# Optimization experiments

Hardware: AMD Instinct MI355X
Metric: run time of the kernel (lower is better)

## Reference

```python
import jax, jax.numpy as jnp
import numpy as np
import math

# Temporal Patch Shift, pattern 'C' (ratio=1 -> all heads shifted).
# torch.roll(x, s, dim=t): out[t] = x[(t - s) % T]
_SHIFT_TABLE_C = np.array([[-4, 1, 2],
                           [-1, 0, 3],
                           [-2, -3, 4]], dtype=np.int32)  # s[i%3, j%3]

def patch_shift_c(feat, inv):
    # feat: (b, T, nW, H, ws, ws, c)
    T, ws = feat.shape[1], feat.shape[4]
    s = jnp.asarray(_SHIFT_TABLE_C)[jnp.arange(ws) % 3][:, jnp.arange(ws) % 3]  # (ws, ws)
    if inv:
        s = -s
    t = jnp.arange(T)
    idx = (t[:, None, None] - s[None, :, :]) % T                 # (T, ws, ws)
    idx = idx[None, :, None, None, :, :, None]                   # bcast to feat rank
    return jnp.take_along_axis(feat, jnp.broadcast_to(idx, feat.shape), axis=1)


def _rel_pos_index(Wd, Wh, Ww):
    coords = np.stack(np.meshgrid(np.arange(Wd), np.arange(Wh), np.arange(Ww), indexing='ij'))
    cf = coords.reshape(3, -1)
    rel = (cf[:, :, None] - cf[:, None, :]).transpose(1, 2, 0).astype(np.int64)
    rel[..., 0] += Wd - 1; rel[..., 1] += Wh - 1; rel[..., 2] += Ww - 1
    rel[..., 0] *= (2 * Wh - 1) * (2 * Ww - 1)
    rel[..., 1] *= (2 * Ww - 1)
    return rel.sum(-1)  # (N, N)


def setup_inputs() -> dict:
    key = jax.random.key(0)
    ks = jax.random.split(key, 5)
    DIM, H = 512, 16
    Wd, Wh, Ww = 1, 7, 7
    N = Wd * Wh * Ww
    B_, bs, fl = 4096, 4, 16  # B_ = bs * fl * 64 windows
    x = jax.random.normal(ks[0], (B_, N, DIM), dtype=jnp.float32)
    qkv_w = jax.random.normal(ks[1], (3 * DIM, DIM), dtype=jnp.float32) * (DIM ** -0.5)
    proj_w = jax.random.normal(ks[2], (DIM, DIM), dtype=jnp.float32) * (DIM ** -0.5)
    proj_b = jnp.zeros((DIM,), dtype=jnp.float32)
    rel_bias_table = jax.random.normal(ks[3], ((2 * Wd - 1) * (2 * Wh - 1) * (2 * Ww - 1), H), dtype=jnp.float32) * 0.02
    rel_index = jnp.asarray(_rel_pos_index(Wd, Wh, Ww), dtype=jnp.int32)
    return {"x": x, "qkv_w": qkv_w, "proj_w": proj_w, "proj_b": proj_b,
            "rel_bias_table": rel_bias_table, "rel_index": rel_index,
            "batch_size": bs, "frame_len": fl}


def reference(x, qkv_w, proj_w, proj_b, rel_bias_table, rel_index, batch_size, frame_len):
    B_, N, C = x.shape
    H = rel_bias_table.shape[-1]
    c = C // H
    ws = int(math.sqrt(N))
    nW = B_ // (batch_size * frame_len)
    scale = c ** -0.5

    qkv = (x @ qkv_w.T).reshape(B_, N, 3, H, c).transpose(2, 0, 3, 1, 4)  # (3, B_, H, N, c)
    q, k, v = qkv[0], qkv[1], qkv[2]

    def shift(t, inv):
        f = t.reshape(batch_size, frame_len, nW, H, ws, ws, c)
        return patch_shift_c(f, inv).reshape(B_, H, N, c)

    q, k, v = shift(q, False), shift(k, False), shift(v, False)

    attn = jnp.einsum('bhnc,bhmc->bhnm', q * scale, k)            # (B_, H, N, N)
    bias = rel_bias_table[rel_index.reshape(-1)].reshape(N, N, H).transpose(2, 0, 1)
    attn = jax.nn.softmax(attn + bias[None], axis=-1)
    out = jnp.einsum('bhnm,bhmc->bhnc', attn, v)                  # (B_, H, N, c)
    out = shift(out, True)                                        # inverse shift back
    out = out.transpose(0, 2, 1, 3).reshape(B_, N, C)
    return out @ proj_w.T + proj_b
```

## Files before the change

kernel.cpp:

```cpp
#include <hip/hip_runtime.h>
#include <stdint.h>

typedef unsigned short u16;
typedef __attribute__((ext_vector_type(8))) short bfrag8;
typedef __attribute__((ext_vector_type(4))) float f32x4;

#define DEV static __device__ __forceinline__

DEV u16 f2bf(float f) {
  uint32_t u = __float_as_uint(f);
  u += 0x7fffu + ((u >> 16) & 1u);
  return (u16)(u >> 16);
}

DEV void async_lds16(const void* g, void* l) {
  const __attribute__((address_space(1))) uint32_t* gp =
      (const __attribute__((address_space(1))) uint32_t*)(uintptr_t)g;
  __attribute__((address_space(3))) uint32_t* lp =
      (__attribute__((address_space(3))) uint32_t*)(uint32_t)(uintptr_t)l;
  __builtin_amdgcn_global_load_lds(gp, lp, 16, 0, 0);
}

DEV int shift_of(int n) {
  int i = n / 7, j = n - i * 7;
  int idx = (i % 3) * 3 + (j % 3);
  return (int)((0x812743650ull >> (4 * idx)) & 15ull) - 4;
}

__global__ void k_f32_to_bf16(const float* __restrict__ src, u16* __restrict__ dst, int n4) {
  int i = blockIdx.x * blockDim.x + threadIdx.x;
  const int stride = gridDim.x * blockDim.x;
  for (; i < n4; i += stride) {
    float4 v = ((const float4*)src)[i];
    union { u16 h[4]; uint2 u; } o;
    o.h[0] = f2bf(v.x); o.h[1] = f2bf(v.y); o.h[2] = f2bf(v.z); o.h[3] = f2bf(v.w);
    ((uint2*)dst)[i] = o.u;
  }
}

__global__ void k_bias_pre(const float* __restrict__ tab, const int* __restrict__ ridx,
                           float* __restrict__ bp) {
  int nm = blockIdx.x * blockDim.x + threadIdx.x;
  if (nm < 2401) {
    int idx = ridx[nm];
#pragma unroll
    for (int h = 0; h < 16; ++h) bp[h * 2401 + nm] = tab[idx * 16 + h];
  }
}

template <int OUT_F32>
__global__ __launch_bounds__(256) void k_gemm_bt(const u16* __restrict__ A,
                                                 const u16* __restrict__ B,
                                                 void* __restrict__ Cp,
                                                 const float* __restrict__ bias,
                                                 int M, int N, int K) {
  __shared__ __align__(16) u16 As[4096];
  __shared__ __align__(16) u16 Bs[4096];
  const int tid = threadIdx.x;
  const int wave = tid >> 6, lane = tid & 63;
  const int quad = lane >> 4, l16 = lane & 15;
  const int wm = ((wave >> 1) & 1) << 6;
  const int wn = (wave & 1) << 6;
  const int bm = blockIdx.x, bn = blockIdx.y;

  f32x4 acc[4][4] = {};

  const int srow = lane >> 2;
  const int scol = (lane & 3) << 3;
  const u16* ga = A + (long)(bm * 128 + srow) * K + scol;
  const u16* gb = B + (long)(bn * 128 + srow) * K + scol;
  const long rstep = (long)16 * K;

  for (int k0 = 0; k0 < K; k0 += 32) {
#pragma unroll
    for (int tt = 0; tt < 2; ++tt) {
      const int region = wave * 2 + tt;
      async_lds16(ga + region * rstep + k0, &As[region * 512]);
      async_lds16(gb + region * rstep + k0, &Bs[region * 512]);
    }
    __syncthreads();
    bfrag8 af[4], bq[4];
#pragma unroll
    for (int mt = 0; mt < 4; ++mt)
      af[mt] = *(const bfrag8*)&As[(wm + mt * 16 + l16) * 32 + quad * 8];
#pragma unroll
    for (int nt = 0; nt < 4; ++nt)
      bq[nt] = *(const bfrag8*)&Bs[(wn + nt * 16 + l16) * 32 + quad * 8];
#pragma unroll
    for (int mt = 0; mt < 4; ++mt)
#pragma unroll
      for (int nt = 0; nt < 4; ++nt)
        acc[mt][nt] = __builtin_amdgcn_mfma_f32_16x16x32_bf16(af[mt], bq[nt], acc[mt][nt], 0, 0, 0);
    __syncthreads();
  }

#pragma unroll
  for (int nt = 0; nt < 4; ++nt) {
    const int col = (bn << 7) + wn + nt * 16 + l16;
    float bv = 0.f;
    if (OUT_F32) bv = bias[col];
#pragma unroll
    for (int mt = 0; mt < 4; ++mt)
#pragma unroll
      for (int i = 0; i < 4; ++i) {
        const long row = (long)(bm << 7) + wm + mt * 16 + quad * 4 + i;
        const float v = acc[mt][nt][i] + bv;
        if (OUT_F32) ((float*)Cp)[row * N + col] = v;
        else         ((u16*)Cp)[row * N + col] = f2bf(v);
      }
  }
}

__global__ __launch_bounds__(256) void k_attn(const u16* __restrict__ qkv,
                                              const float* __restrict__ bias_pre,
                                              u16* __restrict__ out_pre) {
  __shared__ __align__(16) u16 smem[4][6144];
  const int tid = threadIdx.x;
  const int wave = tid >> 6, lane = tid & 63;
  const int quad = lane >> 4, l16 = lane & 15;

  const int unit = (blockIdx.x << 2) + wave;
  const int h = unit & 15;
  const int bflat = unit >> 4;
  const int w = bflat & 63;
  const int t = (bflat >> 6) & 15;
  const int b = bflat >> 10;

  u16* qs = &smem[wave][0];
  u16* ks = &smem[wave][2048];
  u16* vt = &smem[wave][4096];
  u16* ps = &smem[wave][0];

#pragma unroll
  for (int it = 0; it < 8; ++it) {
    int idx = it * 64 + lane;
    vt[(idx >> 4) * 64 + 48 + (idx & 15)] = 0;
  }

  const int r_off = lane >> 2;
  const int ch8 = (lane & 3) << 3;

#pragma unroll
  for (int pass = 0; pass < 4; ++pass) {
    int r = pass * 16 + r_off;
    int rc = r > 48 ? 48 : r;
    int ts = (t - shift_of(rc) + 16) & 15;
    long row = ((long)((b * 16 + ts) * 64 + w)) * 49 + rc;
    const u16* gq = qkv + row * 1536 + h * 32 + ch8;
    async_lds16(gq, qs + pass * 512);
    async_lds16(gq + 512, ks + pass * 512);
  }
#pragma unroll
  for (int pass = 0; pass < 4; ++pass) {
    int r = pass * 16 + r_off;
    if (r < 49) {
      int ts = (t - shift_of(r) + 16) & 15;
      long row = ((long)((b * 16 + ts) * 64 + w)) * 49 + r;
      uint4 d = *(const uint4*)(qkv + row * 1536 + 1024 + h * 32 + ch8);
      const u16* pd = (const u16*)&d;
#pragma unroll
      for (int jj = 0; jj < 8; ++jj) vt[(ch8 + jj) * 64 + r] = pd[jj];
    }
  }

  __builtin_amdgcn_s_waitcnt(0);
  __builtin_amdgcn_sched_barrier(0);

  bfrag8 aq[4], bk[4];
#pragma unroll
  for (int tn = 0; tn < 4; ++tn) aq[tn] = *(const bfrag8*)&qs[(tn * 16 + l16) * 32 + quad * 8];
#pragma unroll
  for (int tm = 0; tm < 4; ++tm) bk[tm] = *(const bfrag8*)&ks[(tm * 16 + l16) * 32 + quad * 8];

  f32x4 s[4][4] = {};
#pragma unroll
  for (int tn = 0; tn < 4; ++tn)
#pragma unroll
    for (int tm = 0; tm < 4; ++tm)
      s[tn][tm] = __builtin_amdgcn_mfma_f32_16x16x32_bf16(aq[tn], bk[tm], s[tn][tm], 0, 0, 0);

  const float scale = 0.17677669529663687f;
#pragma unroll
  for (int tm = 0; tm < 4; ++tm) {
    const int col = tm * 16 + l16;
    const bool valid = col < 49;
    const float* bp = bias_pre + h * 2401 + col;
#pragma unroll
    for (int tn = 0; tn < 4; ++tn)
#pragma unroll
      for (int i = 0; i < 4; ++i) {
        const int row = tn * 16 + quad * 4 + i;
        const int rowc = row > 48 ? 48 : row;
        s[tn][tm][i] = valid ? (s[tn][tm][i] * scale + bp[rowc * 49]) : -1e30f;
      }
  }

  float rinv[4][4];
#pragma unroll
  for (int tn = 0; tn < 4; ++tn) {
#pragma unroll
    for (int i = 0; i < 4; ++i) {
      float m = fmaxf(fmaxf(s[tn][0][i], s[tn][1][i]), fmaxf(s[tn][2][i], s[tn][3][i]));
      m = fmaxf(m, __shfl_xor(m, 1));
      m = fmaxf(m, __shfl_xor(m, 2));
      m = fmaxf(m, __shfl_xor(m, 4));
      m = fmaxf(m, __shfl_xor(m, 8));
      float l = 0.f;
#pragma unroll
      for (int tm = 0; tm < 4; ++tm) {
        float p = __expf(s[tn][tm][i] - m);
        l += p;
        ps[(tn * 16 + quad * 4 + i) * 64 + tm * 16 + l16] = f2bf(p);
      }
      l += __shfl_xor(l, 1);
      l += __shfl_xor(l, 2);
      l += __shfl_xor(l, 4);
      l += __shfl_xor(l, 8);
      rinv[tn][i] = 1.0f / l;
    }
  }

  f32x4 o[4][2] = {};
#pragma unroll
  for (int kt = 0; kt < 2; ++kt) {
    bfrag8 ap[4], bv[2];
#pragma unroll
    for (int tn = 0; tn < 4; ++tn)
      ap[tn] = *(const bfrag8*)&ps[(tn * 16 + l16) * 64 + kt * 32 + quad * 8];
#pragma unroll
    for (int ct = 0; ct < 2; ++ct)
      bv[ct] = *(const bfrag8*)&vt[(ct * 16 + l16) * 64 + kt * 32 + quad * 8];
#pragma unroll
    for (int tn = 0; tn < 4; ++tn)
#pragma unroll
      for (int ct = 0; ct < 2; ++ct)
        o[tn][ct] = __builtin_amdgcn_mfma_f32_16x16x32_bf16(ap[tn], bv[ct], o[tn][ct], 0, 0, 0);
  }

#pragma unroll
  for (int tn = 0; tn < 4; ++tn)
#pragma unroll
    for (int i = 0; i < 4; ++i) {
      const int row = tn * 16 + quad * 4 + i;
      if (row < 49) {
        const int ts = (t - shift_of(row) + 16) & 15;
        const long fd = (long)((b * 16 + ts) * 64 + w);
        const long base = (fd * 49 + row) * 512 + h * 32;
        const float r = rinv[tn][i];
        out_pre[base + l16]      = f2bf(o[tn][0][i] * r);
        out_pre[base + 16 + l16] = f2bf(o[tn][1][i] * r);
      }
    }
}

extern "C" void kernel_launch(void* const* d_in, const int* in_sizes, int n_in,
                              void* d_out, int out_size, void* d_ws, size_t ws_size,
                              hipStream_t stream) {
  const float* x       = (const float*)d_in[0];
  const float* qkv_w   = (const float*)d_in[1];
  const float* proj_w  = (const float*)d_in[2];
  const float* proj_b  = (const float*)d_in[3];
  const float* rel_tab = (const float*)d_in[4];
  const int*   rel_idx = (const int*)d_in[5];

  const long M = 200704;
  char* ws = (char*)d_ws;
  u16*   x_bf     = (u16*)ws;
  u16*   qkvw_bf  = (u16*)(ws + 205520896);
  u16*   projw_bf = (u16*)(ws + 205520896 + 1572864);
  float* bias_pre = (float*)(ws + 205520896 + 1572864 + 524288);
  u16*   qkv_buf  = (u16*)(ws + 205520896 + 1572864 + 524288 + 262144);

  k_f32_to_bf16<<<4096, 256, 0, stream>>>(x, x_bf, (int)(M * 512 / 4));
  k_f32_to_bf16<<<768, 256, 0, stream>>>(qkv_w, qkvw_bf, 1536 * 512 / 4);
  k_f32_to_bf16<<<256, 256, 0, stream>>>(proj_w, projw_bf, 512 * 512 / 4);
  k_bias_pre<<<10, 256, 0, stream>>>(rel_tab, rel_idx, bias_pre);

  dim3 g1(1568, 12);
  k_gemm_bt<0><<<g1, 256, 0, stream>>>(x_bf, qkvw_bf, (void*)qkv_buf, nullptr, (int)M, 1536, 512);

  u16* attn_out = x_bf;
  k_attn<<<16384, 256, 0, stream>>>(qkv_buf, bias_pre, attn_out);

  dim3 g2(1568, 4);
  k_gemm_bt<1><<<g2, 256, 0, stream>>>(attn_out, projw_bf, d_out, proj_b, (int)M, 512, 512);
}
```

Before: 1.897 ms.

## Replace GEMM with 256x256 double-buffered 8-wave pipelined kernel

Replaces the 128x128 single-buffer GEMM used for the QKV and output projections with a 256x256-tile, 512-thread kernel. It uses double-buffered LDS with async global-to-LDS loads interleaved between MFMA phases, an XOR-swizzled LDS layout to avoid bank conflicts, s_setprio around MFMA bursts, and an XCD-aware block remapping. The aim is to hide load latency and raise reuse per LDS byte. In exchange it needs 128 KB of LDS and a large accumulator register footprint, which could limit occupancy.

```diff
diff --git a/kernel.cpp b/kernel.cpp
--- a/kernel.cpp
+++ b/kernel.cpp
@@ -26,6 +26,8 @@
   int idx = (i % 3) * 3 + (j % 3);
   return (int)((0x812743650ull >> (4 * idx)) & 15ull) - 4;
 }
+
+#define FENCE asm volatile("" ::: "memory")
 
 __global__ void k_f32_to_bf16(const float* __restrict__ src, u16* __restrict__ dst, int n4) {
   int i = blockIdx.x * blockDim.x + threadIdx.x;
@@ -48,67 +50,121 @@
   }
 }
 
-template <int OUT_F32>
-__global__ __launch_bounds__(256) void k_gemm_bt(const u16* __restrict__ A,
-                                                 const u16* __restrict__ B,
-                                                 void* __restrict__ Cp,
-                                                 const float* __restrict__ bias,
-                                                 int M, int N, int K) {
-  __shared__ __align__(16) u16 As[4096];
-  __shared__ __align__(16) u16 Bs[4096];
+template <int OUT_F32, int NBN>
+__global__ __launch_bounds__(512, 2) void k_gemm8(const u16* __restrict__ A,
+                                                  const u16* __restrict__ B,
+                                                  void* __restrict__ Cp,
+                                                  const float* __restrict__ bias,
+                                                  int M, int N, int K, int nwg) {
+  (void)M;
+  __shared__ __align__(16) u16 lds[65536];
   const int tid = threadIdx.x;
   const int wave = tid >> 6, lane = tid & 63;
   const int quad = lane >> 4, l16 = lane & 15;
-  const int wm = ((wave >> 1) & 1) << 6;
-  const int wn = (wave & 1) << 6;
-  const int bm = blockIdx.x, bn = blockIdx.y;
-
-  f32x4 acc[4][4] = {};
-
-  const int srow = lane >> 2;
-  const int scol = (lane & 3) << 3;
-  const u16* ga = A + (long)(bm * 128 + srow) * K + scol;
-  const u16* gb = B + (long)(bn * 128 + srow) * K + scol;
-  const long rstep = (long)16 * K;
-
-  for (int k0 = 0; k0 < K; k0 += 32) {
-#pragma unroll
-    for (int tt = 0; tt < 2; ++tt) {
-      const int region = wave * 2 + tt;
-      async_lds16(ga + region * rstep + k0, &As[region * 512]);
-      async_lds16(gb + region * rstep + k0, &Bs[region * 512]);
+  const int wm = wave >> 2, wn = wave & 3;
+
+  const int cpx = nwg >> 3;
+  const int wg = ((int)blockIdx.x & 7) * cpx + ((int)blockIdx.x >> 3);
+  const int bn = wg % NBN, bm = wg / NBN;
+
+  const int r8 = tid >> 3;
+  const int cu = (((tid & 7) ^ (r8 & 7)) << 3);
+  const u16* gA = A + (long)(bm * 256 + r8) * K + cu;
+  const u16* gB = B + (long)(bn * 256 + r8) * K + cu;
+  const long istep = (long)64 * K;
+  const long hstep = (long)128 * K;
+
+#define STAGE_A(t, h) do { const u16* g_ = gA + (h) * hstep + (t) * 64; \
+    u16* l_ = &lds[(((t) & 1) << 15) + ((h) << 13) + (wave << 9)]; \
+    async_lds16(g_, l_); async_lds16(g_ + istep, l_ + 4096); } while (0)
+#define STAGE_B(t, h) do { const u16* g_ = gB + (h) * hstep + (t) * 64; \
+    u16* l_ = &lds[(((t) & 1) << 15) + 16384 + ((h) << 13) + (wave << 9)]; \
+    async_lds16(g_, l_); async_lds16(g_ + istep, l_ + 4096); } while (0)
+
+  const int c0 = (quad << 3) ^ ((l16 & 7) << 3);
+  const int arow = (wm << 6) + l16;
+  const int brow = (wn << 5) + l16;
+
+#define LOADS_A(t, mh) do { const int cb_ = ((t) & 1) << 15; \
+    _Pragma("unroll") for (int a_ = 0; a_ < 4; ++a_) { \
+      const int ro_ = cb_ + ((((mh) << 7) + (a_ << 4) + arow) << 6); \
+      fa[a_ * 2 + 0] = *(const bfrag8*)&lds[ro_ + c0]; \
+      fa[a_ * 2 + 1] = *(const bfrag8*)&lds[ro_ + (c0 ^ 32)]; } } while (0)
+#define LOADS_B(t, nh) do { const int cb_ = (((t) & 1) << 15) + 16384; \
+    _Pragma("unroll") for (int b_ = 0; b_ < 2; ++b_) { \
+      const int ro_ = cb_ + ((((nh) << 7) + (b_ << 4) + brow) << 6); \
+      fb[((nh) * 2 + b_) * 2 + 0] = *(const bfrag8*)&lds[ro_ + c0]; \
+      fb[((nh) * 2 + b_) * 2 + 1] = *(const bfrag8*)&lds[ro_ + (c0 ^ 32)]; } } while (0)
+#define MFMA8(mh, nh) do { \
+    __builtin_amdgcn_s_setprio(1); \
+    _Pragma("unroll") for (int a_ = 0; a_ < 4; ++a_) \
+    _Pragma("unroll") for (int b_ = 0; b_ < 2; ++b_) { \
+      f32x4& c_ = acc[(mh) * 4 + a_][(nh) * 2 + b_]; \
+      c_ = __builtin_amdgcn_mfma_f32_16x16x32_bf16(fa[a_ * 2 + 0], fb[((nh) * 2 + b_) * 2 + 0], c_, 0, 0, 0); \
+      c_ = __builtin_amdgcn_mfma_f32_16x16x32_bf16(fa[a_ * 2 + 1], fb[((nh) * 2 + b_) * 2 + 1], c_, 0, 0, 0); } \
+    __builtin_amdgcn_s_setprio(0); } while (0)
+#define BAR do { FENCE; __builtin_amdgcn_s_barrier(); FENCE; } while (0)
+
+  f32x4 acc[8][4] = {};
+  bfrag8 fa[8], fb[8];
+
+  STAGE_A(0, 0); STAGE_B(0, 0); STAGE_A(0, 1); STAGE_B(0, 1);
+  STAGE_A(1, 0); STAGE_B(1, 0);
+  asm volatile("s_waitcnt vmcnt(4)" ::: "memory");
+  __builtin_amdgcn_s_barrier();
+  FENCE;
+
+  const int nIter = K >> 7;
+  for (int I = 0; I < nIter; ++I) {
+    const int t0 = I * 2, t1 = t0 + 1, t2 = t0 + 2, t3 = t0 + 3;
+    const bool more = (I + 1) < nIter;
+    LOADS_A(t0, 0); LOADS_B(t0, 0);
+    STAGE_A(t1, 1);
+    BAR; MFMA8(0, 0); BAR;
+    LOADS_B(t0, 1);
+    STAGE_B(t1, 1);
+    BAR; MFMA8(0, 1); BAR;
+    LOADS_A(t0, 1);
+    if (more) STAGE_A(t2, 0);
+    BAR; MFMA8(1, 0); BAR;
+    if (more) { STAGE_B(t2, 0); asm volatile("s_waitcnt vmcnt(4)" ::: "memory"); }
+    else      { asm volatile("s_waitcnt vmcnt(0)" ::: "memory"); }
+    BAR; MFMA8(1, 1); BAR;
+    LOADS_A(t1, 0); LOADS_B(t1, 0);
+    if (more) STAGE_A(t2, 1);
+    BAR; MFMA8(0, 0); BAR;
+    LOADS_B(t1, 1);
+    if (more) STAGE_B(t2, 1);
+    BAR; MFMA8(0, 1); BAR;
+    LOADS_A(t1, 1);
+    if (more) STAGE_A(t3, 0);
+    BAR; MFMA8(1, 0); BAR;
+    if (more) { STAGE_B(t3, 0); asm volatile("s_waitcnt vmcnt(4)" ::: "memory"); }
+    BAR; MFMA8(1, 1); BAR;
+  }
+
+#pragma unroll
+  for (int g = 0; g < 4; ++g) {
+    const int col = (bn << 8) + ((g >> 1) << 7) + (wn << 5) + ((g & 1) << 4) + l16;
+    const float bv = OUT_F32 ? bias[col] : 0.0f;
+#pragma unroll
+    for (int f = 0; f < 8; ++f) {
+      const long rb = (long)(bm << 8) + ((f >> 2) << 7) + (wm << 6) + ((f & 3) << 4) + (quad << 2);
+#pragma unroll
+      for (int i = 0; i < 4; ++i) {
+        const float v = acc[f][g][i] + bv;
+        const long off = (rb + i) * N + col;
+        if (OUT_F32) ((float*)Cp)[off] = v;
+        else         ((u16*)Cp)[off] = f2bf(v);
+      }
     }
-    __syncthreads();
-    bfrag8 af[4], bq[4];
-#pragma unroll
-    for (int mt = 0; mt < 4; ++mt)
-      af[mt] = *(const bfrag8*)&As[(wm + mt * 16 + l16) * 32 + quad * 8];
-#pragma unroll
-    for (int nt = 0; nt < 4; ++nt)
-      bq[nt] = *(const bfrag8*)&Bs[(wn + nt * 16 + l16) * 32 + quad * 8];
-#pragma unroll
-    for (int mt = 0; mt < 4; ++mt)
-#pragma unroll
-      for (int nt = 0; nt < 4; ++nt)
-        acc[mt][nt] = __builtin_amdgcn_mfma_f32_16x16x32_bf16(af[mt], bq[nt], acc[mt][nt], 0, 0, 0);
-    __syncthreads();
-  }
-
-#pragma unroll
-  for (int nt = 0; nt < 4; ++nt) {
-    const int col = (bn << 7) + wn + nt * 16 + l16;
-    float bv = 0.f;
-    if (OUT_F32) bv = bias[col];
-#pragma unroll
-    for (int mt = 0; mt < 4; ++mt)
-#pragma unroll
-      for (int i = 0; i < 4; ++i) {
-        const long row = (long)(bm << 7) + wm + mt * 16 + quad * 4 + i;
-        const float v = acc[mt][nt][i] + bv;
-        if (OUT_F32) ((float*)Cp)[row * N + col] = v;
-        else         ((u16*)Cp)[row * N + col] = f2bf(v);
-      }
-  }
+  }
+#undef STAGE_A
+#undef STAGE_B
+#undef LOADS_A
+#undef LOADS_B
+#undef MFMA8
+#undef BAR
 }
 
 __global__ __launch_bounds__(256) void k_attn(const u16* __restrict__ qkv,
@@ -276,12 +332,12 @@
   k_f32_to_bf16<<<256, 256, 0, stream>>>(proj_w, projw_bf, 512 * 512 / 4);
   k_bias_pre<<<10, 256, 0, stream>>>(rel_tab, rel_idx, bias_pre);
 
-  dim3 g1(1568, 12);
-  k_gemm_bt<0><<<g1, 256, 0, stream>>>(x_bf, qkvw_bf, (void*)qkv_buf, nullptr, (int)M, 1536, 512);
+  k_gemm8<0, 6><<<4704, 512, 0, stream>>>(x_bf, qkvw_bf, (void*)qkv_buf, nullptr,
+                                          (int)M, 1536, 512, 4704);
 
   u16* attn_out = x_bf;
   k_attn<<<16384, 256, 0, stream>>>(qkv_buf, bias_pre, attn_out);
 
-  dim3 g2(1568, 4);
-  k_gemm_bt<1><<<g2, 256, 0, stream>>>(attn_out, projw_bf, d_out, proj_b, (int)M, 512, 512);
-}
+  k_gemm8<1, 2><<<1568, 512, 0, stream>>>(attn_out, projw_bf, d_out, proj_b,
+                                          (int)M, 512, 512, 1568);
+}
```

Measured after the change: 1.629 ms. -14.1%, faster.
